# Optimization experiments

Measured on AMD Instinct MI355X. Metric: run time of the kernel, lower is better.

## Reference

```python
import jax, jax.numpy as jnp
import numpy as np


def setup_inputs() -> dict:
    key = jax.random.key(0)
    x = jax.random.normal(key, (2_000_000, 9), dtype=jnp.float32)
    return {"x": x}


def reference(x):
    # Symmetric orthogonalization onto SO(3):
    #   M = U S V^T ;  R = U diag(1, 1, det(U V^T)) V^T
    m = x.reshape(-1, 3, 3)                      # [N, 3, 3]
    u, s, vh = jnp.linalg.svd(m, full_matrices=False)  # u:[N,3,3], vh:[N,3,3] (= V^T)
    det = jnp.linalg.det(jnp.matmul(u, vh))      # [N]
    # Flip last column of U by sign of det to land in SO(3) (det = +1)
    u_fixed = jnp.concatenate(
        [u[:, :, :2], u[:, :, 2:] * det[:, None, None]], axis=2
    )
    return jnp.matmul(u_fixed, vh)               # [N, 3, 3]
```

## Files before the change

kernel.cpp:

```cpp
#include <hip/hip_runtime.h>

#define TPB 256
#define MPW 128
#define FPW (MPW * 9)
#define F4PW (FPW / 4)

typedef float v2f __attribute__((ext_vector_type(2)));
typedef int   v2i __attribute__((ext_vector_type(2)));

static __device__ __forceinline__ v2f sqrt2(v2f a){
    v2f r; r.x = __builtin_amdgcn_sqrtf(a.x); r.y = __builtin_amdgcn_sqrtf(a.y); return r;
}
static __device__ __forceinline__ v2f rsq2(v2f a){
    v2f r; r.x = __builtin_amdgcn_rsqf(a.x); r.y = __builtin_amdgcn_rsqf(a.y); return r;
}
static __device__ __forceinline__ v2f csign2(v2f x, v2f y){
    v2f r; r.x = copysignf(x.x, y.x); r.y = copysignf(x.y, y.y); return r;
}
static __device__ __forceinline__ v2f fabs2(v2f x){
    v2f r; r.x = fabsf(x.x); r.y = fabsf(x.y); return r;
}
static __device__ __forceinline__ v2f sel2(v2i m, v2f a, v2f b){
    v2f r; r.x = m.x ? a.x : b.x; r.y = m.y ? a.y : b.y; return r;
}
static __device__ __forceinline__ void rot2(v2f &p, v2f &q, v2f c, v2f s){
    v2f x = p, y = q; p = c*x - s*y; q = s*x + c*y;
}

static __device__ __forceinline__ void jrot2(v2f &app, v2f &aqq, v2f &apq,
                                             v2f &arp, v2f &arq,
                                             v2f &v0p, v2f &v1p, v2f &v2p,
                                             v2f &v0q, v2f &v1q, v2f &v2q)
{
    v2f d   = aqq - app;
    v2f w   = apq + apq;
    v2f nrm = d*d + w*w;
    v2f rr  = sqrt2(nrm);
    v2f sr  = csign2(rr, d);
    v2f den = d + sr;
    v2f inv = rsq2(den*den + w*w);
    v2f c   = fabs2(den) * inv;
    v2f s   = w * csign2(inv, den);
    v2i tiny = nrm < (v2f)1e-30f;
    c = sel2(tiny, (v2f)1.0f, c);
    s = sel2(tiny, (v2f)0.0f, s);
    v2f sum = app + aqq;
    v2f lo  = 0.5f*(sum - sr);
    app = lo; aqq = sum - lo; apq = (v2f)0.0f;
    rot2(arp, arq, c, s);
    rot2(v0p, v0q, c, s);
    rot2(v1p, v1q, c, s);
    rot2(v2p, v2q, c, s);
}

static __device__ __forceinline__ void solve2(
    v2f m00, v2f m01, v2f m02,
    v2f m10, v2f m11, v2f m12,
    v2f m20, v2f m21, v2f m22,
    v2f &r00, v2f &r01, v2f &r02,
    v2f &r10, v2f &r11, v2f &r12,
    v2f &r20, v2f &r21, v2f &r22)
{
    v2f a00 = m00*m00 + m10*m10 + m20*m20;
    v2f a11 = m01*m01 + m11*m11 + m21*m21;
    v2f a22 = m02*m02 + m12*m12 + m22*m22;
    v2f a01 = m00*m01 + m10*m11 + m20*m21;
    v2f a02 = m00*m02 + m10*m12 + m20*m22;
    v2f a12 = m01*m02 + m11*m12 + m21*m22;

    v2f v00 = (v2f)1.0f, v01 = (v2f)0.0f, v02 = (v2f)0.0f;
    v2f v10 = (v2f)0.0f, v11 = (v2f)1.0f, v12 = (v2f)0.0f;
    v2f v20 = (v2f)0.0f, v21 = (v2f)0.0f, v22 = (v2f)1.0f;

    #pragma unroll
    for (int sw = 0; sw < 3; ++sw) {
        jrot2(a00, a11, a01, a02, a12, v00, v10, v20, v01, v11, v21);
        jrot2(a00, a22, a02, a01, a12, v00, v10, v20, v02, v12, v22);
        jrot2(a11, a22, a12, a01, a02, v01, v11, v21, v02, v12, v22);
    }

    v2f t;
    {
        v2i c01 = a00 < a11;
        t = a00; a00 = sel2(c01, a11, a00); a11 = sel2(c01, t, a11);
        t = v00; v00 = sel2(c01, v01, v00); v01 = sel2(c01, -t, v01);
        t = v10; v10 = sel2(c01, v11, v10); v11 = sel2(c01, -t, v11);
        t = v20; v20 = sel2(c01, v21, v20); v21 = sel2(c01, -t, v21);
    }
    {
        v2i c02 = a00 < a22;
        t = a00; a00 = sel2(c02, a22, a00); a22 = sel2(c02, t, a22);
        t = v00; v00 = sel2(c02, v02, v00); v02 = sel2(c02, -t, v02);
        t = v10; v10 = sel2(c02, v12, v10); v12 = sel2(c02, -t, v12);
        t = v20; v20 = sel2(c02, v22, v20); v22 = sel2(c02, -t, v22);
    }
    {
        v2i c12 = a11 < a22;
        t = a11; a11 = sel2(c12, a22, a11); a22 = sel2(c12, t, a22);
        t = v01; v01 = sel2(c12, v02, v01); v02 = sel2(c12, -t, v02);
        t = v11; v11 = sel2(c12, v12, v11); v12 = sel2(c12, -t, v12);
        t = v21; v21 = sel2(c12, v22, v21); v22 = sel2(c12, -t, v22);
    }

    v2f b00 = m00*v00 + m01*v10 + m02*v20;
    v2f b10 = m10*v00 + m11*v10 + m12*v20;
    v2f b20 = m20*v00 + m21*v10 + m22*v20;
    v2f b01 = m00*v01 + m01*v11 + m02*v21;
    v2f b11 = m10*v01 + m11*v11 + m12*v21;
    v2f b21 = m20*v01 + m21*v11 + m22*v21;

    v2f n1 = b00*b00 + b10*b10 + b20*b20;
    v2f i1 = rsq2(n1);
    v2i ok1 = n1 > (v2f)1e-30f;
    i1 = sel2(ok1, i1, (v2f)0.0f);
    v2f u00 = b00*i1, u10 = b10*i1, u20 = b20*i1;

    v2f d12 = b01*u00 + b11*u10 + b21*u20;
    v2f q0 = b01 - d12*u00;
    v2f q1 = b11 - d12*u10;
    v2f q2 = b21 - d12*u20;
    v2f n2 = q0*q0 + q1*q1 + q2*q2;
    v2f i2 = rsq2(n2);
    v2i ok2 = n2 > (v2f)1e-30f;
    i2 = sel2(ok2, i2, (v2f)0.0f);
    v2f u01 = q0*i2, u11 = q1*i2, u21 = q2*i2;

    v2f u02 = u10*u21 - u20*u11;
    v2f u12 = u20*u01 - u00*u21;
    v2f u22 = u00*u11 - u10*u01;

    r00 = u00*v00 + u01*v01 + u02*v02;
    r01 = u00*v10 + u01*v11 + u02*v12;
    r02 = u00*v20 + u01*v21 + u02*v22;
    r10 = u10*v00 + u11*v01 + u12*v02;
    r11 = u10*v10 + u11*v11 + u12*v12;
    r12 = u10*v20 + u11*v21 + u12*v22;
    r20 = u20*v00 + u21*v01 + u22*v02;
    r21 = u20*v10 + u21*v11 + u22*v12;
    r22 = u20*v20 + u21*v21 + u22*v22;
}

static __device__ __forceinline__ float4 ld_f4(const float* __restrict__ x, long f, long ntotf){
    if (f + 4 <= ntotf) return *(const float4*)(x + f);
    float4 r = make_float4(0.f, 0.f, 0.f, 0.f);
    if (f     < ntotf) r.x = x[f];
    if (f + 1 < ntotf) r.y = x[f + 1];
    if (f + 2 < ntotf) r.z = x[f + 2];
    if (f + 3 < ntotf) r.w = x[f + 3];
    return r;
}
static __device__ __forceinline__ void st_f4(float* __restrict__ o, long f, float4 v, long ntotf){
    if (f + 4 <= ntotf) { *(float4*)(o + f) = v; return; }
    if (f     < ntotf) o[f]     = v.x;
    if (f + 1 < ntotf) o[f + 1] = v.y;
    if (f + 2 < ntotf) o[f + 2] = v.z;
    if (f + 3 < ntotf) o[f + 3] = v.w;
}

__global__ __launch_bounds__(TPB) void svdo_kernel(const float* __restrict__ x,
                                                   float* __restrict__ out,
                                                   int nmat, int ntiles, int W)
{
    __shared__ float lds[4][2 * FPW];
    const int lane = threadIdx.x & 63;
    const int wv   = threadIdx.x >> 6;
    const long ntotf = (long)nmat * 9;

    int tile = blockIdx.x * 4 + wv;
    if (tile >= ntiles) return;

    float* bufA = &lds[wv][0];
    float* bufB = &lds[wv][FPW];

    float4 q0, q1, q2, q3, q4;
    {
        const long fb = (long)tile * FPW;
        q0 = ld_f4(x, fb + (long)(lane       ) * 4, ntotf);
        q1 = ld_f4(x, fb + (long)(lane +  64) * 4, ntotf);
        q2 = ld_f4(x, fb + (long)(lane + 128) * 4, ntotf);
        q3 = ld_f4(x, fb + (long)(lane + 192) * 4, ntotf);
        q4 = make_float4(0.f, 0.f, 0.f, 0.f);
        if (lane < 32) q4 = ld_f4(x, fb + (long)(lane + 256) * 4, ntotf);
    }

    for (;;) {
        *(float4*)&bufA[(lane       ) * 4] = q0;
        *(float4*)&bufA[(lane +  64) * 4] = q1;
        *(float4*)&bufA[(lane + 128) * 4] = q2;
        *(float4*)&bufA[(lane + 192) * 4] = q3;
        if (lane < 32) *(float4*)&bufA[(lane + 256) * 4] = q4;
        asm volatile("s_waitcnt lgkmcnt(0)" ::: "memory");

        const int  nxt  = tile + W;
        const bool have = nxt < ntiles;
        if (have) {
            const long fb = (long)nxt * FPW;
            q0 = ld_f4(x, fb + (long)(lane       ) * 4, ntotf);
            q1 = ld_f4(x, fb + (long)(lane +  64) * 4, ntotf);
            q2 = ld_f4(x, fb + (long)(lane + 128) * 4, ntotf);
            q3 = ld_f4(x, fb + (long)(lane + 192) * 4, ntotf);
            if (lane < 32) q4 = ld_f4(x, fb + (long)(lane + 256) * 4, ntotf);
        }

        {
            const float* p0 = &bufA[lane * 9];
            const float* p1 = &bufA[(lane + 64) * 9];
            v2f m00 = {p0[0], p1[0]}, m01 = {p0[1], p1[1]}, m02 = {p0[2], p1[2]};
            v2f m10 = {p0[3], p1[3]}, m11 = {p0[4], p1[4]}, m12 = {p0[5], p1[5]};
            v2f m20 = {p0[6], p1[6]}, m21 = {p0[7], p1[7]}, m22 = {p0[8], p1[8]};

            v2f r00, r01, r02, r10, r11, r12, r20, r21, r22;
            solve2(m00, m01, m02, m10, m11, m12, m20, m21, m22,
                   r00, r01, r02, r10, r11, r12, r20, r21, r22);

            float* o0 = &bufA[lane * 9];
            o0[0]=r00.x; o0[1]=r01.x; o0[2]=r02.x;
            o0[3]=r10.x; o0[4]=r11.x; o0[5]=r12.x;
            o0[6]=r20.x; o0[7]=r21.x; o0[8]=r22.x;
            float* o1 = &bufA[(lane + 64) * 9];
            o1[0]=r00.y; o1[1]=r01.y; o1[2]=r02.y;
            o1[3]=r10.y; o1[4]=r11.y; o1[5]=r12.y;
            o1[6]=r20.y; o1[7]=r21.y; o1[8]=r22.y;
        }
        asm volatile("s_waitcnt lgkmcnt(0)" ::: "memory");

        {
            const long fb = (long)tile * FPW;
            st_f4(out, fb + (long)(lane       ) * 4, *(const float4*)&bufA[(lane       ) * 4], ntotf);
            st_f4(out, fb + (long)(lane +  64) * 4, *(const float4*)&bufA[(lane +  64) * 4], ntotf);
            st_f4(out, fb + (long)(lane + 128) * 4, *(const float4*)&bufA[(lane + 128) * 4], ntotf);
            st_f4(out, fb + (long)(lane + 192) * 4, *(const float4*)&bufA[(lane + 192) * 4], ntotf);
            if (lane < 32)
                st_f4(out, fb + (long)(lane + 256) * 4, *(const float4*)&bufA[(lane + 256) * 4], ntotf);
        }

        if (!have) break;
        tile = nxt;
        float* ts = bufA; bufA = bufB; bufB = ts;
    }
}

extern "C" void kernel_launch(void* const* d_in, const int* in_sizes, int n_in,
                              void* d_out, int out_size, void* d_ws, size_t ws_size,
                              hipStream_t stream)
{
    (void)n_in; (void)d_ws; (void)ws_size; (void)out_size;
    const float* x = (const float*)d_in[0];
    float* out = (float*)d_out;
    const int nmat = in_sizes[0] / 9;
    const int ntiles = (nmat + MPW - 1) / MPW;
    int grid = (ntiles + 3) / 4;
    if (grid > 1024) grid = 1024;
    const int W = grid * 4;
    svdo_kernel<<<grid, TPB, 0, stream>>>(x, out, nmat, ntiles, W);
}
```

Before: 33.48 us.

## Drop LDS double buffer, add occupancy hint, and double the grid cap

Replaces the per-wave ping-pong LDS buffers with a single buffer, halving shared memory per block from about 36KB to 18KB. It adds a launch-bounds minimum of 8 blocks per CU and raises the grid cap from 1024 to 2048 blocks. The goal is more resident waves to hide memory latency on this bandwidth-bound kernel, at the cost of fewer tiles per wave in the persistent loop and possible register pressure from the occupancy hint. Reusing one buffer looks safe because the prefetch is held in registers and each wave runs in lockstep.

After: 59.72 us. +78.4%, slower.

```diff
diff --git a/kernel.cpp b/kernel.cpp
--- a/kernel.cpp
+++ b/kernel.cpp
@@ -157,11 +157,11 @@
     if (f + 3 < ntotf) o[f + 3] = v.w;
 }
 
-__global__ __launch_bounds__(TPB) void svdo_kernel(const float* __restrict__ x,
-                                                   float* __restrict__ out,
-                                                   int nmat, int ntiles, int W)
-{
-    __shared__ float lds[4][2 * FPW];
+__global__ __launch_bounds__(TPB, 8) void svdo_kernel(const float* __restrict__ x,
+                                                      float* __restrict__ out,
+                                                      int nmat, int ntiles, int W)
+{
+    __shared__ float lds[4][FPW];
     const int lane = threadIdx.x & 63;
     const int wv   = threadIdx.x >> 6;
     const long ntotf = (long)nmat * 9;
@@ -169,8 +169,7 @@
     int tile = blockIdx.x * 4 + wv;
     if (tile >= ntiles) return;
 
-    float* bufA = &lds[wv][0];
-    float* bufB = &lds[wv][FPW];
+    float* L = lds[wv];
 
     float4 q0, q1, q2, q3, q4;
     {
@@ -184,11 +183,11 @@
     }
 
     for (;;) {
-        *(float4*)&bufA[(lane       ) * 4] = q0;
-        *(float4*)&bufA[(lane +  64) * 4] = q1;
-        *(float4*)&bufA[(lane + 128) * 4] = q2;
-        *(float4*)&bufA[(lane + 192) * 4] = q3;
-        if (lane < 32) *(float4*)&bufA[(lane + 256) * 4] = q4;
+        *(float4*)&L[(lane       ) * 4] = q0;
+        *(float4*)&L[(lane +  64) * 4] = q1;
+        *(float4*)&L[(lane + 128) * 4] = q2;
+        *(float4*)&L[(lane + 192) * 4] = q3;
+        if (lane < 32) *(float4*)&L[(lane + 256) * 4] = q4;
         asm volatile("s_waitcnt lgkmcnt(0)" ::: "memory");
 
         const int  nxt  = tile + W;
@@ -203,8 +202,8 @@
         }
 
         {
-            const float* p0 = &bufA[lane * 9];
-            const float* p1 = &bufA[(lane + 64) * 9];
+            const float* p0 = &L[lane * 9];
+            const float* p1 = &L[(lane + 64) * 9];
             v2f m00 = {p0[0], p1[0]}, m01 = {p0[1], p1[1]}, m02 = {p0[2], p1[2]};
             v2f m10 = {p0[3], p1[3]}, m11 = {p0[4], p1[4]}, m12 = {p0[5], p1[5]};
             v2f m20 = {p0[6], p1[6]}, m21 = {p0[7], p1[7]}, m22 = {p0[8], p1[8]};
@@ -213,11 +212,11 @@
             solve2(m00, m01, m02, m10, m11, m12, m20, m21, m22,
                    r00, r01, r02, r10, r11, r12, r20, r21, r22);
 
-            float* o0 = &bufA[lane * 9];
+            float* o0 = &L[lane * 9];
             o0[0]=r00.x; o0[1]=r01.x; o0[2]=r02.x;
             o0[3]=r10.x; o0[4]=r11.x; o0[5]=r12.x;
             o0[6]=r20.x; o0[7]=r21.x; o0[8]=r22.x;
-            float* o1 = &bufA[(lane + 64) * 9];
+            float* o1 = &L[(lane + 64) * 9];
             o1[0]=r00.y; o1[1]=r01.y; o1[2]=r02.y;
             o1[3]=r10.y; o1[4]=r11.y; o1[5]=r12.y;
             o1[6]=r20.y; o1[7]=r21.y; o1[8]=r22.y;
@@ -226,17 +225,16 @@
 
         {
             const long fb = (long)tile * FPW;
-            st_f4(out, fb + (long)(lane       ) * 4, *(const float4*)&bufA[(lane       ) * 4], ntotf);
-            st_f4(out, fb + (long)(lane +  64) * 4, *(const float4*)&bufA[(lane +  64) * 4], ntotf);
-            st_f4(out, fb + (long)(lane + 128) * 4, *(const float4*)&bufA[(lane + 128) * 4], ntotf);
-            st_f4(out, fb + (long)(lane + 192) * 4, *(const float4*)&bufA[(lane + 192) * 4], ntotf);
+            st_f4(out, fb + (long)(lane       ) * 4, *(const float4*)&L[(lane       ) * 4], ntotf);
+            st_f4(out, fb + (long)(lane +  64) * 4, *(const float4*)&L[(lane +  64) * 4], ntotf);
+            st_f4(out, fb + (long)(lane + 128) * 4, *(const float4*)&L[(lane + 128) * 4], ntotf);
+            st_f4(out, fb + (long)(lane + 192) * 4, *(const float4*)&L[(lane + 192) * 4], ntotf);
             if (lane < 32)
-                st_f4(out, fb + (long)(lane + 256) * 4, *(const float4*)&bufA[(lane + 256) * 4], ntotf);
+                st_f4(out, fb + (long)(lane + 256) * 4, *(const float4*)&L[(lane + 256) * 4], ntotf);
         }
 
         if (!have) break;
         tile = nxt;
-        float* ts = bufA; bufA = bufB; bufB = ts;
     }
 }
 
@@ -250,7 +248,7 @@
     const int nmat = in_sizes[0] / 9;
     const int ntiles = (nmat + MPW - 1) / MPW;
     int grid = (ntiles + 3) / 4;
-    if (grid > 1024) grid = 1024;
+    if (grid > 2048) grid = 2048;
     const int W = grid * 4;
     svdo_kernel<<<grid, TPB, 0, stream>>>(x, out, nmat, ntiles, W);
 }
```
